# Kernel optimization log

Measured on AMD Instinct MI355X. Metric: run time of the kernel, lower is better.

The kernel has to match this reference:

```python
import jax, jax.numpy as jnp
import numpy as np

A = 1.0  # slope of hard sigmoid (init arg `a`)


def setup_inputs() -> dict:
    key = jax.random.key(0)
    ks = jax.random.split(key, 10)
    H, B, BOT, TOP = 1024, 4096, 1024, 1024
    stdv = 1.0 / np.sqrt(H)
    u = lambda k, shp: jax.random.uniform(k, shp, jnp.float32, -stdv, stdv)
    U_11 = u(ks[0], (4 * H + 1, H))
    U_21 = u(ks[1], (4 * H + 1, TOP))
    W_01 = u(ks[2], (4 * H + 1, BOT))
    bias = u(ks[3], (4 * H + 1,))
    c = jax.random.normal(ks[4], (H, B), jnp.float32) * 0.1
    h = jnp.tanh(jax.random.normal(ks[5], (H, B), jnp.float32))
    h_bottom = jnp.tanh(jax.random.normal(ks[6], (BOT, B), jnp.float32))
    h_top = jnp.tanh(jax.random.normal(ks[7], (TOP, B), jnp.float32))
    z = (jax.random.uniform(ks[8], (1, B)) > 0.5).astype(jnp.float32)
    z_bottom = (jax.random.uniform(ks[9], (1, B)) > 0.5).astype(jnp.float32)
    return dict(c=c, h_bottom=h_bottom, h=h, h_top=h_top, z=z,
                z_bottom=z_bottom, U_11=U_11, U_21=U_21, W_01=W_01, bias=bias)


def reference(c, h_bottom, h, h_top, z, z_bottom, U_11, U_21, W_01, bias):
    H = U_11.shape[1]
    # [4H+1, B] pre-activations: recurrent + gated top-down + gated bottom-up + bias
    f_s = (W_01 @ h_bottom
           + z * (U_21 @ h_top)
           + z_bottom * (U_11 @ h)
           + bias[:, None])
    f = jax.nn.sigmoid(f_s[0:H])
    i = jax.nn.sigmoid(f_s[H:2 * H])
    o = jax.nn.sigmoid(f_s[2 * H:3 * H])
    g = jnp.tanh(f_s[3 * H:4 * H])
    z_hat = jnp.clip((f_s[4 * H:4 * H + 1] * A + 1.0) / 2.0, 0.0, 1.0)  # hard_sigm
    one = 1.0
    c_new = (z * (i * g)
             + (one - z) * (one - z_bottom) * c
             + (one - z) * z_bottom * (f * c + i * g))
    tanh_c = jnp.tanh(c_new)
    h_new = (z * o * tanh_c
             + (one - z) * (one - z_bottom) * h
             + (one - z) * z_bottom * o * tanh_c)
    # straight-through binary boundary: forward step(z_hat>0.5), backward identity
    z_new = z_hat + jax.lax.stop_gradient((z_hat > 0.5).astype(z_hat.dtype) - z_hat)
    return h_new, c_new, z_new
```

## Files before the change

### kernel.cpp

```cpp
#include <hip/hip_runtime.h>
#include <hip/hip_bf16.h>
#include <math.h>

#define Hd   1024
#define Bsz  4096
#define Kc   3072
#define NTt  96
#define CH   512

typedef unsigned short u16;
typedef __attribute__((ext_vector_type(8))) u16 u16x8;
typedef __attribute__((ext_vector_type(4))) float f32x4;
typedef __attribute__((ext_vector_type(8))) short bf16x8;

__device__ inline u16 f2bf(float f) {
    __hip_bfloat16 h = __float2bfloat16(f);
    return *reinterpret_cast<u16*>(&h);
}

__device__ inline float sigm(float x) { return 1.0f / (1.0f + __expf(-x)); }

__device__ inline void gload16(const void* g, const void* s) {
    __builtin_amdgcn_global_load_lds(
        (const __attribute__((address_space(1))) void*)g,
        (__attribute__((address_space(3))) void*)s, 16, 0, 0);
}

#define BAR()   __builtin_amdgcn_s_barrier()
#define VMW(n)  asm volatile("s_waitcnt vmcnt(" #n ")" ::: "memory")
#define PRIO1() __builtin_amdgcn_s_setprio(1)
#define PRIO0() __builtin_amdgcn_s_setprio(0)


__global__ __launch_bounds__(256) void prep_A(const float* __restrict__ U11,
                                              const float* __restrict__ U21,
                                              const float* __restrict__ W01,
                                              u16* __restrict__ Ab,
                                              float* __restrict__ out) {
    __shared__ u16 lds[16 * 520];
    if (blockIdx.x == 0 && blockIdx.y == 0) {
        float* outz = out + (size_t)2 * Hd * Bsz;
        for (int i = threadIdx.x; i < Bsz; i += 256) outz[i] = 0.0f;
    }
    const int mb = blockIdx.x, kb = blockIdx.y;
    const int t = threadIdx.x;
    const int r16 = t >> 4, j = t & 15;
    const int row = mb * 16 + r16, gate = row & 3, r = row >> 2;
    const int sel = kb >> 1;
    const int k0 = (kb & 1) * 512 + j * 32;
    const float* src = (sel == 0) ? W01 : ((sel == 1) ? U21 : U11);
    const float4* p = reinterpret_cast<const float4*>(
        src + ((size_t)(gate * Hd + r)) * Hd + k0);
#pragma unroll
    for (int g = 0; g < 4; ++g) {
        float4 v0 = p[g * 2], v1 = p[g * 2 + 1];
        u16x8 o;
        o[0] = f2bf(v0.x); o[1] = f2bf(v0.y); o[2] = f2bf(v0.z); o[3] = f2bf(v0.w);
        o[4] = f2bf(v1.x); o[5] = f2bf(v1.y); o[6] = f2bf(v1.z); o[7] = f2bf(v1.w);
        *reinterpret_cast<u16x8*>(&lds[j * 520 + (g * 16 + r16) * 8]) = o;
    }
    __syncthreads();
    const int c = t >> 4, jj = t & 15;
    u16* gdst = Ab + ((size_t)(mb * NTt + kb * 16 + c)) * CH;
#pragma unroll
    for (int i = 0; i < 4; ++i)
        *reinterpret_cast<u16x8*>(gdst + i * 128 + jj * 8) =
            *reinterpret_cast<const u16x8*>(&lds[c * 520 + i * 128 + jj * 8]);
}

__global__ __launch_bounds__(256) void prep_B(const float* __restrict__ hb,
                                              const float* __restrict__ ht,
                                              const float* __restrict__ hh,
                                              const float* __restrict__ z,
                                              const float* __restrict__ zb,
                                              const float* __restrict__ U11,
                                              const float* __restrict__ U21,
                                              const float* __restrict__ W01,
                                              u16* __restrict__ Bb,
                                              float* __restrict__ out) {
    __shared__ float tile[64][33];
    __shared__ float red[8][32];
    const int n0 = blockIdx.x * 32;
    const int kg0 = blockIdx.y * 64;
    const int sel = kg0 >> 10;
    const int k0 = kg0 & 1023;
    const float* src = (sel == 0) ? hb : ((sel == 1) ? ht : hh);
    const float* wsrc = (sel == 0) ? W01 : ((sel == 1) ? U21 : U11);
    const int t = threadIdx.x, tx = t & 31, ty = t >> 5;
#pragma unroll
    for (int j = 0; j < 8; ++j) {
        int kk = ty * 8 + j;
        tile[kk][tx] = src[(size_t)(k0 + kk) * Bsz + n0 + tx];
    }
    __syncthreads();
    {
        const int c = t >> 6, l = t & 63, g = l >> 4, n16 = l & 15;
        const int kt_loc = c & 1, nb_loc = c >> 1;
        const int nl = nb_loc * 16 + n16;
        const int n = n0 + nl;
        const float s = (sel == 0) ? 1.0f : ((sel == 1) ? z[n] : zb[n]);
        u16x8 o;
#pragma unroll
        for (int e = 0; e < 8; ++e)
            o[e] = f2bf(tile[kt_loc * 32 + g * 8 + e][nl] * s);
        const int nb = (n0 >> 4) + nb_loc, kt = (kg0 >> 5) + kt_loc;
        *reinterpret_cast<u16x8*>(Bb + ((size_t)(nb * NTt + kt)) * CH +
                                  (g * 16 + n16) * 8) = o;
    }
    {
        int col = t & 31, seg = t >> 5;
        const float* w = wsrc + (size_t)4096 * 1024 + k0 + seg * 8;
        float p = 0.0f;
#pragma unroll
        for (int j = 0; j < 8; ++j) p += w[j] * tile[seg * 8 + j][col];
        red[seg][col] = p;
        __syncthreads();
        if (seg == 0) {
            float tot = 0.0f;
#pragma unroll
            for (int q = 0; q < 8; ++q) tot += red[q][col];
            int n = n0 + col;
            float sca = (sel == 0) ? 1.0f : ((sel == 1) ? z[n] : zb[n]);
            atomicAdd(out + (size_t)2 * Hd * Bsz + n, tot * sca);
        }
    }
}

__global__ __launch_bounds__(512, 4) void gemm_fused(
    const u16* __restrict__ A, const u16* __restrict__ Bm,
    const float* __restrict__ c_in, const float* __restrict__ h_in,
    const float* __restrict__ z, const float* __restrict__ zb,
    const float* __restrict__ bias, float* __restrict__ out) {
    extern __shared__ __align__(16) u16 smem[];
    u16* const As = smem;
    u16* const Bs = smem + 16384;

    const int t = threadIdx.x;
    const int w = t >> 6, l = t & 63;
    const int wm = w >> 2, wn = w & 3;
    const int fr = l & 15, fq = l >> 4;

    const int orig = blockIdx.x;
    const int wg = ((orig & 7) << 6) | (orig >> 3);
    const int bm = wg >> 5, bn = wg & 31;

    f32x4 acc[8][2];
#pragma unroll
    for (int i = 0; i < 8; ++i)
#pragma unroll
        for (int j = 0; j < 2; ++j) acc[i][j] = (f32x4){0.f, 0.f, 0.f, 0.f};

    auto stageA = [&](int buf, int kt) {
#pragma unroll
        for (int iss = 0; iss < 2; ++iss) {
            int mb = bm * 16 + iss * 8 + w;
            gload16(A + ((size_t)(mb * NTt + kt)) * CH + l * 8,
                    As + buf * 8192 + iss * 4096 + w * 512 + l * 8);
        }
    };
    auto stageB = [&](int buf, int kt) {
        int nb = bn * 8 + w;
        gload16(Bm + ((size_t)(nb * NTt + kt)) * CH + l * 8,
                Bs + buf * 4096 + w * 512 + l * 8);
    };

    stageA(0, 0); stageB(0, 0);

    for (int T = 0; T < NTt; ++T) {
        const int p = T & 1;
        if (T + 1 < NTt) {
            stageA(p ^ 1, T + 1); stageB(p ^ 1, T + 1);
            VMW(3);
        } else {
            VMW(0);
        }
        BAR();
        const u16* Ap = As + p * 8192;
        const u16* Bpp = Bs + p * 4096;
        bf16x8 bF0 = *reinterpret_cast<const bf16x8*>(Bpp + (wn * 2 + 0) * CH + l * 8);
        bf16x8 bF1 = *reinterpret_cast<const bf16x8*>(Bpp + (wn * 2 + 1) * CH + l * 8);
        PRIO1();
#pragma unroll
        for (int h2 = 0; h2 < 2; ++h2) {
            bf16x8 a0 = *reinterpret_cast<const bf16x8*>(Ap + (wm * 8 + h2 * 4 + 0) * CH + l * 8);
            bf16x8 a1 = *reinterpret_cast<const bf16x8*>(Ap + (wm * 8 + h2 * 4 + 1) * CH + l * 8);
            bf16x8 a2 = *reinterpret_cast<const bf16x8*>(Ap + (wm * 8 + h2 * 4 + 2) * CH + l * 8);
            bf16x8 a3 = *reinterpret_cast<const bf16x8*>(Ap + (wm * 8 + h2 * 4 + 3) * CH + l * 8);
            acc[h2 * 4 + 0][0] = __builtin_amdgcn_mfma_f32_16x16x32_bf16(a0, bF0, acc[h2 * 4 + 0][0], 0, 0, 0);
            acc[h2 * 4 + 0][1] = __builtin_amdgcn_mfma_f32_16x16x32_bf16(a0, bF1, acc[h2 * 4 + 0][1], 0, 0, 0);
            acc[h2 * 4 + 1][0] = __builtin_amdgcn_mfma_f32_16x16x32_bf16(a1, bF0, acc[h2 * 4 + 1][0], 0, 0, 0);
            acc[h2 * 4 + 1][1] = __builtin_amdgcn_mfma_f32_16x16x32_bf16(a1, bF1, acc[h2 * 4 + 1][1], 0, 0, 0);
            acc[h2 * 4 + 2][0] = __builtin_amdgcn_mfma_f32_16x16x32_bf16(a2, bF0, acc[h2 * 4 + 2][0], 0, 0, 0);
            acc[h2 * 4 + 2][1] = __builtin_amdgcn_mfma_f32_16x16x32_bf16(a2, bF1, acc[h2 * 4 + 2][1], 0, 0, 0);
            acc[h2 * 4 + 3][0] = __builtin_amdgcn_mfma_f32_16x16x32_bf16(a3, bF0, acc[h2 * 4 + 3][0], 0, 0, 0);
            acc[h2 * 4 + 3][1] = __builtin_amdgcn_mfma_f32_16x16x32_bf16(a3, bF1, acc[h2 * 4 + 3][1], 0, 0, 0);
        }
        PRIO0();
        BAR();
    }

    float zc[2], zbv[2];
#pragma unroll
    for (int ni = 0; ni < 2; ++ni) {
        int n = bn * 128 + wn * 32 + ni * 16 + fr;
        zc[ni] = z[n]; zbv[ni] = zb[n];
    }
#pragma unroll
    for (int mi = 0; mi < 8; ++mi) {
        const int r = bm * 64 + wm * 32 + mi * 4 + fq;
        const float b0 = bias[r], b1 = bias[Hd + r];
        const float b2 = bias[2 * Hd + r], b3 = bias[3 * Hd + r];
        const float* crow = c_in + (size_t)r * Bsz;
        const float* hrow = h_in + (size_t)r * Bsz;
        float* hout = out + (size_t)r * Bsz;
        float* cout = out + (size_t)Hd * Bsz + (size_t)r * Bsz;
#pragma unroll
        for (int ni = 0; ni < 2; ++ni) {
            const int n = bn * 128 + wn * 32 + ni * 16 + fr;
            f32x4 a = acc[mi][ni];
            float co = crow[n], ho = hrow[n];
            float fg = sigm(a[0] + b0);
            float ig = sigm(a[1] + b1);
            float og = sigm(a[2] + b2);
            float gg = tanhf(a[3] + b3);
            float i_g = ig * gg;
            float nz = 1.0f - zc[ni], nzb = 1.0f - zbv[ni];
            float cn = zc[ni] * i_g + nz * nzb * co + nz * zbv[ni] * (fg * co + i_g);
            float tc2 = tanhf(cn);
            float hn = zc[ni] * og * tc2 + nz * nzb * ho + nz * zbv[ni] * og * tc2;
            hout[n] = hn; cout[n] = cn;
        }
    }

    if (bm == 0 && t < 128) {
        float* outz = out + (size_t)2 * Hd * Bsz;
        int n = bn * 128 + t;
        float s = outz[n] + bias[4096];
        float zh = (s + 1.0f) * 0.5f;
        zh = fminf(fmaxf(zh, 0.0f), 1.0f);
        outz[n] = (zh > 0.5f) ? 1.0f : 0.0f;
    }
}

extern "C" void kernel_launch(void* const* d_in, const int* in_sizes, int n_in,
                              void* d_out, int out_size, void* d_ws, size_t ws_size,
                              hipStream_t stream) {
    (void)in_sizes; (void)n_in; (void)out_size; (void)ws_size;
    const float* c    = (const float*)d_in[0];
    const float* hb   = (const float*)d_in[1];
    const float* h    = (const float*)d_in[2];
    const float* ht   = (const float*)d_in[3];
    const float* z    = (const float*)d_in[4];
    const float* zb   = (const float*)d_in[5];
    const float* U11  = (const float*)d_in[6];
    const float* U21  = (const float*)d_in[7];
    const float* W01  = (const float*)d_in[8];
    const float* bias = (const float*)d_in[9];
    float* out = (float*)d_out;

    u16* Ab = (u16*)d_ws;
    u16* Bb = Ab + (size_t)256 * NTt * CH;

    hipFuncSetAttribute(reinterpret_cast<const void*>(gemm_fused),
                        hipFuncAttributeMaxDynamicSharedMemorySize, 49152);

    prep_A<<<dim3(256, 6), 256, 0, stream>>>(U11, U21, W01, Ab, out);
    prep_B<<<dim3(128, 48), 256, 0, stream>>>(hb, ht, h, z, zb, U11, U21, W01, Bb, out);
    gemm_fused<<<512, 512, 49152, stream>>>(Ab, Bb, c, h, z, zb, bias, out);
}
```

Before: 123.3 us.

## Use 4 waves per block with larger 8x4 MFMA tiles per wave

```diff
diff --git a/kernel.cpp b/kernel.cpp
--- a/kernel.cpp
+++ b/kernel.cpp
@@ -126,7 +126,7 @@
     }
 }
 
-__global__ __launch_bounds__(512, 4) void gemm_fused(
+__global__ __launch_bounds__(256, 2) void gemm_fused(
     const u16* __restrict__ A, const u16* __restrict__ Bm,
     const float* __restrict__ c_in, const float* __restrict__ h_in,
     const float* __restrict__ z, const float* __restrict__ zb,
@@ -137,31 +137,31 @@
 
     const int t = threadIdx.x;
     const int w = t >> 6, l = t & 63;
-    const int wm = w >> 2, wn = w & 3;
+    const int wm = w >> 1, wn = w & 1;
     const int fr = l & 15, fq = l >> 4;
 
     const int orig = blockIdx.x;
     const int wg = ((orig & 7) << 6) | (orig >> 3);
     const int bm = wg >> 5, bn = wg & 31;
 
-    f32x4 acc[8][2];
+    f32x4 acc[8][4];
 #pragma unroll
     for (int i = 0; i < 8; ++i)
 #pragma unroll
-        for (int j = 0; j < 2; ++j) acc[i][j] = (f32x4){0.f, 0.f, 0.f, 0.f};
-
+        for (int j = 0; j < 4; ++j) acc[i][j] = (f32x4){0.f, 0.f, 0.f, 0.f};
+
+    const int tc = t >> 6, te = t & 63;
     auto stageA = [&](int buf, int kt) {
 #pragma unroll
-        for (int iss = 0; iss < 2; ++iss) {
-            int mb = bm * 16 + iss * 8 + w;
-            gload16(A + ((size_t)(mb * NTt + kt)) * CH + l * 8,
-                    As + buf * 8192 + iss * 4096 + w * 512 + l * 8);
-        }
+        for (int i = 0; i < 4; ++i)
+            gload16(A + ((size_t)((bm * 16 + i * 4 + tc) * NTt + kt)) * CH + te * 8,
+                    As + buf * 8192 + i * 2048 + t * 8);
     };
     auto stageB = [&](int buf, int kt) {
-        int nb = bn * 8 + w;
-        gload16(Bm + ((size_t)(nb * NTt + kt)) * CH + l * 8,
-                Bs + buf * 4096 + w * 512 + l * 8);
+#pragma unroll
+        for (int i = 0; i < 2; ++i)
+            gload16(Bm + ((size_t)((bn * 8 + i * 4 + tc) * NTt + kt)) * CH + te * 8,
+                    Bs + buf * 4096 + i * 2048 + t * 8);
     };
 
     stageA(0, 0); stageB(0, 0);
@@ -170,53 +170,49 @@
         const int p = T & 1;
         if (T + 1 < NTt) {
             stageA(p ^ 1, T + 1); stageB(p ^ 1, T + 1);
-            VMW(3);
+            VMW(6);
         } else {
             VMW(0);
         }
         BAR();
         const u16* Ap = As + p * 8192;
-        const u16* Bpp = Bs + p * 4096;
-        bf16x8 bF0 = *reinterpret_cast<const bf16x8*>(Bpp + (wn * 2 + 0) * CH + l * 8);
-        bf16x8 bF1 = *reinterpret_cast<const bf16x8*>(Bpp + (wn * 2 + 1) * CH + l * 8);
+        const u16* Bp = Bs + p * 4096;
+        bf16x8 aF[8], bF[4];
+#pragma unroll
+        for (int mi = 0; mi < 8; ++mi)
+            aF[mi] = *reinterpret_cast<const bf16x8*>(Ap + (wm * 8 + mi) * CH + l * 8);
+#pragma unroll
+        for (int ni = 0; ni < 4; ++ni)
+            bF[ni] = *reinterpret_cast<const bf16x8*>(Bp + (wn * 4 + ni) * CH + l * 8);
         PRIO1();
 #pragma unroll
-        for (int h2 = 0; h2 < 2; ++h2) {
-            bf16x8 a0 = *reinterpret_cast<const bf16x8*>(Ap + (wm * 8 + h2 * 4 + 0) * CH + l * 8);
-            bf16x8 a1 = *reinterpret_cast<const bf16x8*>(Ap + (wm * 8 + h2 * 4 + 1) * CH + l * 8);
-            bf16x8 a2 = *reinterpret_cast<const bf16x8*>(Ap + (wm * 8 + h2 * 4 + 2) * CH + l * 8);
-            bf16x8 a3 = *reinterpret_cast<const bf16x8*>(Ap + (wm * 8 + h2 * 4 + 3) * CH + l * 8);
-            acc[h2 * 4 + 0][0] = __builtin_amdgcn_mfma_f32_16x16x32_bf16(a0, bF0, acc[h2 * 4 + 0][0], 0, 0, 0);
-            acc[h2 * 4 + 0][1] = __builtin_amdgcn_mfma_f32_16x16x32_bf16(a0, bF1, acc[h2 * 4 + 0][1], 0, 0, 0);
-            acc[h2 * 4 + 1][0] = __builtin_amdgcn_mfma_f32_16x16x32_bf16(a1, bF0, acc[h2 * 4 + 1][0], 0, 0, 0);
-            acc[h2 * 4 + 1][1] = __builtin_amdgcn_mfma_f32_16x16x32_bf16(a1, bF1, acc[h2 * 4 + 1][1], 0, 0, 0);
-            acc[h2 * 4 + 2][0] = __builtin_amdgcn_mfma_f32_16x16x32_bf16(a2, bF0, acc[h2 * 4 + 2][0], 0, 0, 0);
-            acc[h2 * 4 + 2][1] = __builtin_amdgcn_mfma_f32_16x16x32_bf16(a2, bF1, acc[h2 * 4 + 2][1], 0, 0, 0);
-            acc[h2 * 4 + 3][0] = __builtin_amdgcn_mfma_f32_16x16x32_bf16(a3, bF0, acc[h2 * 4 + 3][0], 0, 0, 0);
-            acc[h2 * 4 + 3][1] = __builtin_amdgcn_mfma_f32_16x16x32_bf16(a3, bF1, acc[h2 * 4 + 3][1], 0, 0, 0);
-        }
+        for (int mi = 0; mi < 8; ++mi)
+#pragma unroll
+            for (int ni = 0; ni < 4; ++ni)
+                acc[mi][ni] = __builtin_amdgcn_mfma_f32_16x16x32_bf16(
+                    aF[mi], bF[ni], acc[mi][ni], 0, 0, 0);
         PRIO0();
         BAR();
     }
 
-    float zc[2], zbv[2];
-#pragma unroll
-    for (int ni = 0; ni < 2; ++ni) {
-        int n = bn * 128 + wn * 32 + ni * 16 + fr;
+    float zc[4], zbv[4];
+#pragma unroll
+    for (int ni = 0; ni < 4; ++ni) {
+        int n = bn * 128 + wn * 64 + ni * 16 + fr;
         zc[ni] = z[n]; zbv[ni] = zb[n];
     }
 #pragma unroll
     for (int mi = 0; mi < 8; ++mi) {
-        const int r = bm * 64 + wm * 32 + mi * 4 + fq;
-        const float b0 = bias[r], b1 = bias[Hd + r];
-        const float b2 = bias[2 * Hd + r], b3 = bias[3 * Hd + r];
-        const float* crow = c_in + (size_t)r * Bsz;
-        const float* hrow = h_in + (size_t)r * Bsz;
-        float* hout = out + (size_t)r * Bsz;
-        float* cout = out + (size_t)Hd * Bsz + (size_t)r * Bsz;
-#pragma unroll
-        for (int ni = 0; ni < 2; ++ni) {
-            const int n = bn * 128 + wn * 32 + ni * 16 + fr;
+        const int u = bm * 64 + wm * 32 + mi * 4 + fq;
+        const float b0 = bias[u], b1 = bias[Hd + u];
+        const float b2 = bias[2 * Hd + u], b3 = bias[3 * Hd + u];
+        const float* crow = c_in + (size_t)u * Bsz;
+        const float* hrow = h_in + (size_t)u * Bsz;
+        float* hout = out + (size_t)u * Bsz;
+        float* cout = out + (size_t)Hd * Bsz + (size_t)u * Bsz;
+#pragma unroll
+        for (int ni = 0; ni < 4; ++ni) {
+            const int n = bn * 128 + wn * 64 + ni * 16 + fr;
             f32x4 a = acc[mi][ni];
             float co = crow[n], ho = hrow[n];
             float fg = sigm(a[0] + b0);
@@ -266,5 +262,5 @@
 
     prep_A<<<dim3(256, 6), 256, 0, stream>>>(U11, U21, W01, Ab, out);
     prep_B<<<dim3(128, 48), 256, 0, stream>>>(hb, ht, h, z, zb, U11, U21, W01, Bb, out);
-    gemm_fused<<<512, 512, 49152, stream>>>(Ab, Bb, c, h, z, zb, bias, out);
-}
+    gemm_fused<<<512, 256, 49152, stream>>>(Ab, Bb, c, h, z, zb, bias, out);
+}
```

New measurement: 120.3 us. -2.5%, faster.
